# Performance work log

Hardware: AMD Instinct MI355X
Metric: run time of the kernel (lower is better)

## Reference

```python
import jax, jax.numpy as jnp
import numpy as np

B, C, H, W = 8, 64, 112, 112
F, KH, KW = 128, 3, 3
SPARSITY = 0.7  # fraction of kernel entries zeroed (Uniform connector)


def setup_inputs() -> dict:
    key = jax.random.key(0)
    k1, k2, k3 = jax.random.split(key, 3)
    inputs = jax.random.normal(k1, (B, C, H, W), dtype=jnp.float32)
    fan_in = C * KH * KW
    limit = float(np.sqrt(6.0 / (F + fan_in)))
    vals = jax.random.uniform(k2, (F, fan_in), minval=-limit, maxval=limit, dtype=jnp.float32)
    mask = (jax.random.uniform(k3, (F, fan_in)) >= SPARSITY).astype(jnp.float32)
    kernel = vals * mask  # dense representation of the sparse kernel
    return {"inputs": inputs, "kernel": kernel}


def _extract_patches(x, kh, kw):
    # x: [B, S1, S2, C]; VALID padding, stride 1, rate 1.
    # Matches tf.image.extract_patches depth ordering: (pi, pj) major, channel minor.
    Bb, S1, S2, Cc = x.shape
    o1, o2 = S1 - kh + 1, S2 - kw + 1
    pats = jnp.stack(
        [x[:, i:i + o1, j:j + o2, :] for i in range(kh) for j in range(kw)],
        axis=3,
    )  # [B, o1, o2, kh*kw, C]
    return pats.reshape(Bb, o1, o2, kh * kw * Cc)


def reference(inputs, kernel):
    # inputs: [B, C, H, W] (NCHW, per bias_add data_format and build())
    x = jnp.transpose(inputs, (0, 3, 2, 1))  # [B, W, H, C] (perm [0,3,2,1] in original)
    p = _extract_patches(x, KH, KW)          # [B, oW, oH, KH*KW*C]
    # spmm(kernel [F, K], im2col [K, B*oW*oH]) expressed as a single contraction
    out = jnp.einsum('bwhk,fk->bfwh', p, kernel)  # [B, F, oW, oH]
    return out
```

## Files before the change

### kernel.cpp

```cpp
#include <hip/hip_runtime.h>

typedef unsigned short u16;
typedef unsigned int u32;
typedef _Float16 f16x8 __attribute__((ext_vector_type(8)));
typedef float f32x16 __attribute__((ext_vector_type(16)));

#define B_ 8
#define C_ 64
#define H_ 112
#define W_ 112
#define HW_ 12544
#define F_ 128
#define OH_ 110
#define OW_ 110
#define OWOH 12100
#define NPOS 96800
#define KK_ 576
#define NT_ 384
#define NWGF 506
#define OCTSTRIDE 802816
#define AELEMS 73728
#define AHALF 36864

__device__ __forceinline__ void gl_lds16(const void* g, void* l) {
  __builtin_amdgcn_global_load_lds((const __attribute__((address_space(1))) void*)g,
                                   (__attribute__((address_space(3))) void*)l,
                                   16, 0, 0);
}

__global__ __launch_bounds__(256) void prep_all(const float* __restrict__ in,
                                                const float* __restrict__ k,
                                                u16* __restrict__ xT,
                                                u16* __restrict__ kT) {
  const int bid = blockIdx.x;
  const int tid = threadIdx.x;
  if (bid >= 896) {
    const int base = (bid - 896) * 2048;
#pragma unroll
    for (int t = 0; t < 8; ++t) {
      int idx = base + t * 256 + tid;
      int c = idx & 7;
      int f = (idx >> 3) & 127;
      int hf = (idx >> 10) & 1;
      int ko16 = idx >> 11;
      _Float16 h = (_Float16)k[f * KK_ + ko16 * 16 + hf * 8 + c];
      kT[idx] = __builtin_bit_cast(u16, h);
    }
    return;
  }
  __shared__ float tile[8][8][113];
  const int b = bid / 112;
  const int r = bid % 112;
  const int oct = r / 14;
  const int hs = (r % 14) * 8;

  for (int idx = tid; idx < 8 * 8 * 112; idx += 256) {
    int c = idx / 896;
    int rem = idx - c * 896;
    int h = rem / 112;
    int w = rem - h * 112;
    tile[c][h][w] = in[(((size_t)(b * 64 + oct * 8 + c)) * 112 + (hs + h)) * 112 + w];
  }
  __syncthreads();

  for (int idx = tid; idx < 896; idx += 256) {
    int w = idx >> 3;
    int h = idx & 7;
    f16x8 v;
#pragma unroll
    for (int c = 0; c < 8; ++c) v[c] = (_Float16)tile[c][h][w];
    size_t o = ((((size_t)oct * B_ + b) * W_ + w) * H_ + (hs + h)) * 8;
    *(f16x8*)(xT + o) = v;
  }
}

__global__ __launch_bounds__(256, 2) void conv_mfma(
    const u16* __restrict__ xT, const u16* __restrict__ kT,
    float* __restrict__ out) {
  __shared__ u16 lds[AHALF];

  const int tid = threadIdx.x;
  const int wave = tid >> 6;
  const int lane = tid & 63;
  const int l31 = lane & 31;
  const int hi = lane >> 5;

  const int orig = blockIdx.x;
  const int xcd = orig & 7;
  const int sub = orig >> 3;
  const int wg = (xcd < 2 ? xcd * 64 : 128 + (xcd - 2) * 63) + sub;
  const int nblk = wg >> 1;
  const int fh = wg & 1;
  const int n0 = nblk * NT_ + wave * 96;

  int posOff[3];
#pragma unroll
  for (int ni = 0; ni < 3; ++ni) {
    int n = n0 + ni * 32 + l31;
    if (n >= NPOS) n = 0;
    int b = n / OWOH;
    int r = n - b * OWOH;
    int w = r / OH_;
    int h = r - w * OH_;
    posOff[ni] = ((b * W_ + w) * H_ + h) * 8;
  }

  f16x8 b0[6];
#pragma unroll
  for (int ni = 0; ni < 3; ++ni)
#pragma unroll
    for (int t = 0; t < 2; ++t)
      b0[ni * 2 + t] = *(const f16x8*)(xT + (t * 2 + hi) * OCTSTRIDE + posOff[ni]);

#pragma unroll
  for (int it = 0; it < 18; ++it) {
    const int m = it * 256 + tid;
    const int src = ((m >> 6) << 7) + (fh << 6) + (m & 63);
    gl_lds16(kT + src * 8, (char*)lds + m * 16);
  }
  __syncthreads();

  f32x16 acc[2][3] = {};

#pragma unroll
  for (int s = 0; s < 18; ++s) {
    const int tap = s >> 1;
    const int half = s & 1;
    const int i = tap / 3;
    const int j = tap - i * 3;
    const int sShift = (i * H_ + j) * 8;

    f16x8 bh[6];
    if (s == 0) {
#pragma unroll
      for (int q = 0; q < 6; ++q) bh[q] = b0[q];
    } else {
#pragma unroll
      for (int ni = 0; ni < 3; ++ni)
#pragma unroll
        for (int t = 0; t < 2; ++t)
          bh[ni * 2 + t] = *(const f16x8*)(xT + (half * 4 + t * 2 + hi) * OCTSTRIDE +
                                           posOff[ni] + sShift);
    }

    f16x8 ah[4];
#pragma unroll
    for (int t = 0; t < 2; ++t)
#pragma unroll
      for (int mi = 0; mi < 2; ++mi)
        ah[t * 2 + mi] = *(const f16x8*)&lds[((((s * 2 + t) * 2 + hi) << 6) + mi * 32 + l31) * 8];

#pragma unroll
    for (int t = 0; t < 2; ++t)
#pragma unroll
      for (int mi = 0; mi < 2; ++mi)
#pragma unroll
        for (int ni = 0; ni < 3; ++ni)
          acc[mi][ni] = __builtin_amdgcn_mfma_f32_32x32x16_f16(ah[t * 2 + mi], bh[ni * 2 + t],
                                                               acc[mi][ni], 0, 0, 0);
  }

#pragma unroll
  for (int ni = 0; ni < 3; ++ni) {
    int n = n0 + ni * 32 + l31;
    if (n >= NPOS) continue;
    int b = n / OWOH;
    int r = n - b * OWOH;
    int w = r / OH_;
    int h = r - w * OH_;
    float* op = out + ((size_t)(b * F_) * OW_ + w) * OH_ + h;
#pragma unroll
    for (int mi = 0; mi < 2; ++mi) {
      const int fbase = fh * 64 + mi * 32 + 4 * hi;
#pragma unroll
      for (int reg = 0; reg < 16; ++reg) {
        int f = fbase + (reg & 3) + 8 * (reg >> 2);
        op[(size_t)f * OWOH] = acc[mi][ni][reg];
      }
    }
  }
}

__global__ void naive_conv(const float* __restrict__ in, const float* __restrict__ ker,
                           float* __restrict__ out) {
  int idx = blockIdx.x * 256 + threadIdx.x;
  const int total = B_ * F_ * OW_ * OH_;
  if (idx >= total) return;
  int h = idx % OH_;
  int w = (idx / OH_) % OW_;
  int f = (idx / (OW_ * OH_)) % F_;
  int b = idx / (F_ * OW_ * OH_);
  float s = 0.f;
  for (int tap = 0; tap < 9; ++tap) {
    int i = tap / 3, j = tap % 3;
    const float* ip = in + ((size_t)b * C_ * H_ + (h + j)) * W_ + (w + i);
    const float* kp = ker + (size_t)f * KK_ + tap * C_;
    for (int c = 0; c < C_; ++c) s += ip[(size_t)c * HW_] * kp[c];
  }
  out[idx] = s;
}

extern "C" void kernel_launch(void* const* d_in, const int* in_sizes, int n_in,
                              void* d_out, int out_size, void* d_ws, size_t ws_size,
                              hipStream_t stream) {
  const float* in = (const float*)d_in[0];
  const float* ker = (const float*)d_in[1];
  float* out = (float*)d_out;

  const size_t xElems = (size_t)B_ * H_ * W_ * C_;
  const size_t need = (xElems + AELEMS) * 2;

  if (ws_size < need) {
    int total = B_ * F_ * OW_ * OH_;
    naive_conv<<<(total + 255) / 256, 256, 0, stream>>>(in, ker, out);
    return;
  }

  u16* xT = (u16*)d_ws;
  u16* kT = xT + xElems;

  prep_all<<<932, 256, 0, stream>>>(in, ker, xT, kT);
  conv_mfma<<<NWGF, 256, 0, stream>>>(xT, kT, out);
}
```

Measured before the change: 38.80 us.

## Split filter dimension into quarters per workgroup to raise occupancy

Each workgroup now computes 32 filters instead of 64, so twice as many workgroups are launched, each with half the LDS and half the accumulators, and the launch bound allows 4 blocks per CU. The XCD-aware block remapping and the early prefetch of the first input tile (overlapped with the LDS weight load) are dropped. This aims for more parallelism and latency hiding, but every input patch is now read from global/L2 by four workgroups instead of two, doubling activation traffic per MFMA.

```diff
diff --git a/kernel.cpp b/kernel.cpp
--- a/kernel.cpp
+++ b/kernel.cpp
@@ -17,10 +17,10 @@
 #define NPOS 96800
 #define KK_ 576
 #define NT_ 384
-#define NWGF 506
+#define NWGQ 1012
 #define OCTSTRIDE 802816
 #define AELEMS 73728
-#define AHALF 36864
+#define AQUAR 18432
 
 __device__ __forceinline__ void gl_lds16(const void* g, void* l) {
   __builtin_amdgcn_global_load_lds((const __attribute__((address_space(1))) void*)g,
@@ -74,10 +74,10 @@
   }
 }
 
-__global__ __launch_bounds__(256, 2) void conv_mfma(
+__global__ __launch_bounds__(256, 4) void conv_mfma(
     const u16* __restrict__ xT, const u16* __restrict__ kT,
     float* __restrict__ out) {
-  __shared__ u16 lds[AHALF];
+  __shared__ u16 lds[AQUAR];
 
   const int tid = threadIdx.x;
   const int wave = tid >> 6;
@@ -85,12 +85,9 @@
   const int l31 = lane & 31;
   const int hi = lane >> 5;
 
-  const int orig = blockIdx.x;
-  const int xcd = orig & 7;
-  const int sub = orig >> 3;
-  const int wg = (xcd < 2 ? xcd * 64 : 128 + (xcd - 2) * 63) + sub;
-  const int nblk = wg >> 1;
-  const int fh = wg & 1;
+  const int wg = blockIdx.x;
+  const int nblk = wg >> 2;
+  const int fq = wg & 3;
   const int n0 = nblk * NT_ + wave * 96;
 
   int posOff[3];
@@ -105,22 +102,15 @@
     posOff[ni] = ((b * W_ + w) * H_ + h) * 8;
   }
 
-  f16x8 b0[6];
-#pragma unroll
-  for (int ni = 0; ni < 3; ++ni)
-#pragma unroll
-    for (int t = 0; t < 2; ++t)
-      b0[ni * 2 + t] = *(const f16x8*)(xT + (t * 2 + hi) * OCTSTRIDE + posOff[ni]);
-
-#pragma unroll
-  for (int it = 0; it < 18; ++it) {
+#pragma unroll
+  for (int it = 0; it < 9; ++it) {
     const int m = it * 256 + tid;
-    const int src = ((m >> 6) << 7) + (fh << 6) + (m & 63);
+    const int src = ((m >> 5) << 7) + (fq << 5) + (m & 31);
     gl_lds16(kT + src * 8, (char*)lds + m * 16);
   }
   __syncthreads();
 
-  f32x16 acc[2][3] = {};
+  f32x16 acc[3] = {};
 
 #pragma unroll
   for (int s = 0; s < 18; ++s) {
@@ -131,33 +121,23 @@
     const int sShift = (i * H_ + j) * 8;
 
     f16x8 bh[6];
-    if (s == 0) {
-#pragma unroll
-      for (int q = 0; q < 6; ++q) bh[q] = b0[q];
-    } else {
+#pragma unroll
+    for (int ni = 0; ni < 3; ++ni)
+#pragma unroll
+      for (int t = 0; t < 2; ++t)
+        bh[ni * 2 + t] = *(const f16x8*)(xT + (half * 4 + t * 2 + hi) * OCTSTRIDE +
+                                         posOff[ni] + sShift);
+
+    f16x8 ah[2];
+#pragma unroll
+    for (int t = 0; t < 2; ++t)
+      ah[t] = *(const f16x8*)&lds[((((s * 2 + t) * 2 + hi) << 5) + l31) * 8];
+
+#pragma unroll
+    for (int t = 0; t < 2; ++t)
 #pragma unroll
       for (int ni = 0; ni < 3; ++ni)
-#pragma unroll
-        for (int t = 0; t < 2; ++t)
-          bh[ni * 2 + t] = *(const f16x8*)(xT + (half * 4 + t * 2 + hi) * OCTSTRIDE +
-                                           posOff[ni] + sShift);
-    }
-
-    f16x8 ah[4];
-#pragma unroll
-    for (int t = 0; t < 2; ++t)
-#pragma unroll
-      for (int mi = 0; mi < 2; ++mi)
-        ah[t * 2 + mi] = *(const f16x8*)&lds[((((s * 2 + t) * 2 + hi) << 6) + mi * 32 + l31) * 8];
-
-#pragma unroll
-    for (int t = 0; t < 2; ++t)
-#pragma unroll
-      for (int mi = 0; mi < 2; ++mi)
-#pragma unroll
-        for (int ni = 0; ni < 3; ++ni)
-          acc[mi][ni] = __builtin_amdgcn_mfma_f32_32x32x16_f16(ah[t * 2 + mi], bh[ni * 2 + t],
-                                                               acc[mi][ni], 0, 0, 0);
+        acc[ni] = __builtin_amdgcn_mfma_f32_32x32x16_f16(ah[t], bh[ni * 2 + t], acc[ni], 0, 0, 0);
   }
 
 #pragma unroll
@@ -169,14 +149,11 @@
     int w = r / OH_;
     int h = r - w * OH_;
     float* op = out + ((size_t)(b * F_) * OW_ + w) * OH_ + h;
-#pragma unroll
-    for (int mi = 0; mi < 2; ++mi) {
-      const int fbase = fh * 64 + mi * 32 + 4 * hi;
-#pragma unroll
-      for (int reg = 0; reg < 16; ++reg) {
-        int f = fbase + (reg & 3) + 8 * (reg >> 2);
-        op[(size_t)f * OWOH] = acc[mi][ni][reg];
-      }
+    const int fbase = fq * 32 + 4 * hi;
+#pragma unroll
+    for (int reg = 0; reg < 16; ++reg) {
+      int f = fbase + (reg & 3) + 8 * (reg >> 2);
+      op[(size_t)f * OWOH] = acc[ni][reg];
     }
   }
 }
@@ -220,5 +197,5 @@
   u16* kT = xT + xElems;
 
   prep_all<<<932, 256, 0, stream>>>(in, ker, xT, kT);
-  conv_mfma<<<NWGF, 256, 0, stream>>>(xT, kT, out);
-}
+  conv_mfma<<<NWGQ, 256, 0, stream>>>(xT, kT, out);
+}
```

Result: slower. 83.82 us (+116.0%).
